# Optimization experiments

Hardware: AMD Instinct MI355X
Metric: run time of the kernel (lower is better)

The kernel has to match this reference:

```python
import jax, jax.numpy as jnp
import numpy as np

B, T, D_IN, D_H, D_OUT = 256, 512, 512, 1024, 512


def setup_inputs() -> dict:
    key = jax.random.key(0)
    k_x, k_wfc, k_bfc, k_wo, k_bo = jax.random.split(key, 5)
    # PyTorch Linear default init: U(-1/sqrt(fan_in), 1/sqrt(fan_in))
    lim_fc = 1.0 / np.sqrt(D_IN + D_H)
    lim_out = 1.0 / np.sqrt(D_H)
    return {
        "x": jax.random.normal(k_x, (B, T, D_IN), dtype=jnp.float32),
        "h": jnp.zeros((B, D_H), dtype=jnp.float32),
        "W_fc": jax.random.uniform(k_wfc, (D_H, D_IN + D_H), jnp.float32, -lim_fc, lim_fc),
        "b_fc": jax.random.uniform(k_bfc, (D_H,), jnp.float32, -lim_fc, lim_fc),
        "W_out": jax.random.uniform(k_wo, (D_OUT, D_H), jnp.float32, -lim_out, lim_out),
        "b_out": jax.random.uniform(k_bo, (D_OUT,), jnp.float32, -lim_out, lim_out),
    }


def reference(x, h, W_fc, b_fc, W_out, b_out):
    # x: [B, T, D_in], h: [B, D_h]
    xT = jnp.swapaxes(x, 0, 1)  # [T, B, D_in] for scan over time

    def step(h_t, x_t):
        combined = jnp.concatenate([x_t, h_t], axis=-1)  # [B, D_in + D_h]
        h_new = jnp.tanh(combined @ W_fc.T + b_fc)
        return h_new, None

    h_final, _ = jax.lax.scan(step, h, xT)
    y = h_final @ W_out.T + b_out  # [B, D_out]
    return (y, h_final)
```

## Files before the change

kernel.cpp:

```cpp
#include <hip/hip_runtime.h>
#include <hip/hip_bf16.h>
#include <math.h>

#define RNN_B    256
#define RNN_T    512
#define RNN_DIN  512
#define RNN_DH   1024
#define RNN_DOUT 512
#define RNN_K    (RNN_DIN + RNN_DH)

#define NGRP 16
#define MR   16
#define NBLK 16
#define NC   64

typedef __bf16 bf16x8 __attribute__((ext_vector_type(8)));
typedef float  f32x4  __attribute__((ext_vector_type(4)));
typedef unsigned long long u64;
typedef unsigned int u32;
typedef unsigned short u16;

static __device__ __forceinline__ bf16x8 ld_bf8(const __hip_bfloat16* p) {
  return *reinterpret_cast<const bf16x8*>(p);
}

static __device__ __forceinline__ bf16x8 ld_f32_as_bf8(const float* p) {
  const float4* q = reinterpret_cast<const float4*>(p);
  float4 u = q[0], v = q[1];
  bf16x8 r;
  r[0] = (__bf16)u.x; r[1] = (__bf16)u.y; r[2] = (__bf16)u.z; r[3] = (__bf16)u.w;
  r[4] = (__bf16)v.x; r[5] = (__bf16)v.y; r[6] = (__bf16)v.z; r[7] = (__bf16)v.w;
  return r;
}

__global__ void cast_f32_to_bf16(const float* __restrict__ src,
                                 unsigned long long* __restrict__ dst,
                                 int n4) {
  int i = blockIdx.x * blockDim.x + threadIdx.x;
  const int stride = gridDim.x * blockDim.x;
  for (; i < n4; i += stride) {
    float4 v = reinterpret_cast<const float4*>(src)[i];
    unsigned long long w =
        (unsigned long long)__builtin_bit_cast(unsigned short, (__bf16)v.x)
      | ((unsigned long long)__builtin_bit_cast(unsigned short, (__bf16)v.y) << 16)
      | ((unsigned long long)__builtin_bit_cast(unsigned short, (__bf16)v.z) << 32)
      | ((unsigned long long)__builtin_bit_cast(unsigned short, (__bf16)v.w) << 48);
    dst[i] = w;
  }
}

template<bool USE_XBF>
static __device__ __forceinline__ void xpart(const __hip_bfloat16* xbf, const float* xf,
                                             const __hip_bfloat16* Wbf,
                                             int m0, int nw, int lm, int lk, int t,
                                             f32x4* acc) {
#pragma unroll
  for (int i = 0; i < 4; ++i) acc[i] = (f32x4){0.f, 0.f, 0.f, 0.f};
  const __hip_bfloat16* Wr = Wbf + (size_t)(nw + lm) * RNN_K + lk;
  if constexpr (USE_XBF) {
    const __hip_bfloat16* xb = xbf + ((size_t)(m0 + lm) * RNN_T + (t - 1)) * RNN_DIN + lk;
#pragma unroll
    for (int s = 0; s < 16; ++s) {
      bf16x8 a = ld_bf8(xb + s * 32);
      bf16x8 b = ld_bf8(Wr + s * 32);
      acc[s & 3] = __builtin_amdgcn_mfma_f32_16x16x32_bf16(a, b, acc[s & 3], 0, 0, 0);
    }
  } else {
    const float* xb = xf + ((size_t)(m0 + lm) * RNN_T + (t - 1)) * RNN_DIN + lk;
#pragma unroll
    for (int s = 0; s < 16; ++s) {
      bf16x8 a = ld_f32_as_bf8(xb + s * 32);
      bf16x8 b = ld_bf8(Wr + s * 32);
      acc[s & 3] = __builtin_amdgcn_mfma_f32_16x16x32_bf16(a, b, acc[s & 3], 0, 0, 0);
    }
  }
}

template<bool USE_XBF>
__launch_bounds__(256, 1)
__global__ void rnn_scan(const __hip_bfloat16* __restrict__ xbf,
                         const float* __restrict__ xf,
                         const __hip_bfloat16* __restrict__ Wbf,
                         const float* __restrict__ bfc,
                         u32* hbuf32,
                         unsigned int* flags,
                         float* __restrict__ outh)
{
  const int bid = blockIdx.x;
  const int g = bid >> 4;
  const int c = bid & 15;
  const int tid = threadIdx.x;
  const int w  = tid >> 6;
  const int l  = tid & 63;
  const int lm = l & 15;
  const int lk = (l >> 4) * 8;
  const int m0 = g * MR;
  const int nw = c * NC + w * 16;

  __shared__ __align__(16) u32 hls[MR * 516];
  __shared__ __align__(16) u16 ots[16 * 68];

  const float bv = bfc[nw + lm];
  const int rr = (l >> 4) * 4;
  unsigned int* myflags = flags + g * (RNN_T + 1);
  const __hip_bfloat16* Wrh = Wbf + (size_t)(nw + lm) * RNN_K + RNN_DIN + lk;

  f32x4 acc[4];
  xpart<USE_XBF>(xbf, xf, Wbf, m0, nw, lm, lk, 1, acc);

  for (int t = 1; t <= RNN_T; ++t) {
    if (t > 1) {
      if (tid == 0) {
        unsigned int* fp = myflags + (t - 1);
        int it = 0;
        while (__hip_atomic_load(fp, __ATOMIC_RELAXED, __HIP_MEMORY_SCOPE_AGENT)
               < (unsigned)NBLK) {
          __builtin_amdgcn_s_sleep(1);
          if (++it > 4000000) break;
        }
      }
      __syncthreads();
    }

    {
      const u32* hsrc = hbuf32 + (size_t)((t - 1) & 1) * 131072 + (size_t)m0 * 512;
      u32 stg[32];
#pragma unroll
      for (int i = 0; i < 32; ++i)
        stg[i] = __hip_atomic_load(hsrc + i * 256 + tid,
                                   __ATOMIC_RELAXED, __HIP_MEMORY_SCOPE_AGENT);
#pragma unroll
      for (int i = 0; i < 32; ++i) {
        const int n = i * 256 + tid;
        hls[(n >> 9) * 516 + (n & 511)] = stg[i];
      }
    }
    __syncthreads();

#pragma unroll
    for (int ks = 0; ks < 32; ++ks) {
      const bf16x8 a = *reinterpret_cast<const bf16x8*>(
          &hls[lm * 516 + ks * 16 + (l >> 4) * 4]);
      const bf16x8 b = ld_bf8(Wrh + ks * 32);
      acc[ks & 3] = __builtin_amdgcn_mfma_f32_16x16x32_bf16(a, b, acc[ks & 3], 0, 0, 0);
    }

#pragma unroll
    for (int q = 0; q < 4; ++q) {
      float s = acc[0][q] + acc[1][q] + acc[2][q] + acc[3][q] + bv;
      float e  = __expf(-2.0f * fabsf(s));
      float th = (1.0f - e) * __builtin_amdgcn_rcpf(1.0f + e);
      float v  = copysignf(th, s);
      ots[(rr + q) * 68 + w * 16 + lm] = __builtin_bit_cast(u16, (__bf16)v);
      if (t == RNN_T) outh[(size_t)(m0 + rr + q) * RNN_DH + nw + lm] = v;
    }
    __syncthreads();

    {
      const u32* ots32 = reinterpret_cast<const u32*>(ots);
      const int i = tid >> 4, j0 = (tid & 15) * 2;
      u32 v0 = ots32[i * 34 + j0];
      u32 v1 = ots32[i * 34 + j0 + 1];
      u32* hdst = hbuf32 + (size_t)(t & 1) * 131072 + (size_t)(m0 + i) * 512 + c * 32;
      u32 r0 = __hip_atomic_exchange(hdst + j0,     v0,
                                     __ATOMIC_RELAXED, __HIP_MEMORY_SCOPE_AGENT);
      u32 r1 = __hip_atomic_exchange(hdst + j0 + 1, v1,
                                     __ATOMIC_RELAXED, __HIP_MEMORY_SCOPE_AGENT);
      asm volatile("" :: "v"(r0), "v"(r1));
    }
    asm volatile("s_waitcnt vmcnt(0)" ::: "memory");
    __syncthreads();

    if (tid == 0)
      __hip_atomic_fetch_add(myflags + t, 1u,
                             __ATOMIC_RELAXED, __HIP_MEMORY_SCOPE_AGENT);

    if (t < RNN_T) xpart<USE_XBF>(xbf, xf, Wbf, m0, nw, lm, lk, t + 1, acc);
  }
}

__global__ void out_gemm_mfma(const __hip_bfloat16* __restrict__ hfin,
                              const __hip_bfloat16* __restrict__ Wob,
                              const float* __restrict__ bout,
                              float* __restrict__ y)
{
  const int mi = blockIdx.x >> 3;
  const int ni = blockIdx.x & 7;
  const int w = threadIdx.x >> 6, l = threadIdx.x & 63;
  const int lm = l & 15, lk = (l >> 4) * 8;
  const int row0 = mi * 64 + w * 16;
  const int col0 = ni * 64;

  f32x4 acc[4];
#pragma unroll
  for (int i = 0; i < 4; ++i) acc[i] = (f32x4){0.f, 0.f, 0.f, 0.f};

#pragma unroll 4
  for (int ks = 0; ks < 32; ++ks) {
    bf16x8 a = ld_bf8(hfin + (size_t)(row0 + lm) * RNN_DH + ks * 32 + lk);
#pragma unroll
    for (int nf = 0; nf < 4; ++nf) {
      bf16x8 b = ld_bf8(Wob + (size_t)(col0 + nf * 16 + lm) * RNN_DH + ks * 32 + lk);
      acc[nf] = __builtin_amdgcn_mfma_f32_16x16x32_bf16(a, b, acc[nf], 0, 0, 0);
    }
  }
  const int rr = (l >> 4) * 4;
#pragma unroll
  for (int nf = 0; nf < 4; ++nf)
#pragma unroll
    for (int q = 0; q < 4; ++q)
      y[(size_t)(row0 + rr + q) * RNN_DOUT + col0 + nf * 16 + lm] =
          acc[nf][q] + bout[col0 + nf * 16 + lm];
}

__global__ void out_gemm(const float* __restrict__ hfin, const float* __restrict__ Wout,
                         const float* __restrict__ bout, float* __restrict__ y) {
  __shared__ float hs[RNN_DH];
  const int b = blockIdx.x;
  for (int j = threadIdx.x; j < RNN_DH; j += 256)
    hs[j] = hfin[(size_t)b * RNN_DH + j];
  __syncthreads();
  for (int o = threadIdx.x; o < RNN_DOUT; o += 256) {
    const float4* wr = reinterpret_cast<const float4*>(Wout + (size_t)o * RNN_DH);
    float acc = 0.f;
#pragma unroll 4
    for (int k4 = 0; k4 < RNN_DH / 4; ++k4) {
      float4 wv = wr[k4];
      acc += hs[4*k4] * wv.x + hs[4*k4+1] * wv.y + hs[4*k4+2] * wv.z + hs[4*k4+3] * wv.w;
    }
    y[(size_t)b * RNN_DOUT + o] = acc + bout[o];
  }
}

extern "C" void kernel_launch(void* const* d_in, const int* in_sizes, int n_in,
                              void* d_out, int out_size, void* d_ws, size_t ws_size,
                              hipStream_t stream) {
  const float* x    = (const float*)d_in[0];
  const float* h0   = (const float*)d_in[1];
  const float* Wfc  = (const float*)d_in[2];
  const float* bfc  = (const float*)d_in[3];
  const float* Wout = (const float*)d_in[4];
  const float* bout = (const float*)d_in[5];

  float* y    = (float*)d_out;
  float* outh = y + (size_t)RNN_B * RNN_DOUT;

  char* p = (char*)d_ws;
  __hip_bfloat16* hbuf = (__hip_bfloat16*)p;  p += (size_t)2 * RNN_B * RNN_DH * 2;
  unsigned int*   flags = (unsigned int*)p;   p += 65536;
  __hip_bfloat16* Wbf  = (__hip_bfloat16*)p;  p += (size_t)RNN_DH * RNN_K * 2;
  __hip_bfloat16* Wob  = (__hip_bfloat16*)p;
  const size_t need_wob = (size_t)(p - (char*)d_ws) + (size_t)RNN_DOUT * RNN_DH * 2;
  p += (size_t)RNN_DOUT * RNN_DH * 2;
  __hip_bfloat16* xbf  = (__hip_bfloat16*)p;
  const size_t need_xbf = (size_t)(p - (char*)d_ws) + (size_t)RNN_B * RNN_T * RNN_DIN * 2;
  const bool use_wob = (ws_size >= need_wob);
  const bool use_xbf = (ws_size >= need_xbf);

  hipMemsetAsync(flags, 0, NGRP * (RNN_T + 1) * sizeof(unsigned int), stream);

  cast_f32_to_bf16<<<dim3(1024), dim3(256), 0, stream>>>(
      Wfc, (unsigned long long*)Wbf, RNN_DH * RNN_K / 4);
  cast_f32_to_bf16<<<dim3(256), dim3(256), 0, stream>>>(
      h0, (unsigned long long*)hbuf, RNN_B * RNN_DH / 4);
  if (use_wob)
    cast_f32_to_bf16<<<dim3(256), dim3(256), 0, stream>>>(
        Wout, (unsigned long long*)Wob, RNN_DOUT * RNN_DH / 4);
  if (use_xbf)
    cast_f32_to_bf16<<<dim3(2048), dim3(256), 0, stream>>>(
        x, (unsigned long long*)xbf, RNN_B * RNN_T * RNN_DIN / 4);

  u32* hbuf32 = (u32*)hbuf;
  void* kargs[] = { (void*)&xbf, (void*)&x, (void*)&Wbf, (void*)&bfc,
                    (void*)&hbuf32, (void*)&flags, (void*)&outh };
  if (use_xbf) {
    hipLaunchCooperativeKernel((const void*)&rnn_scan<true>,
                               dim3(256), dim3(256), kargs, 0, stream);
  } else {
    hipLaunchCooperativeKernel((const void*)&rnn_scan<false>,
                               dim3(256), dim3(256), kargs, 0, stream);
  }

  if (use_wob) {
    out_gemm_mfma<<<dim3(32), dim3(256), 0, stream>>>(hbuf, Wob, bout, y);
  } else {
    out_gemm<<<dim3(256), dim3(256), 0, stream>>>(outh, Wout, bout, y);
  }
}
```

Measured before the change: 3.204 ms.

## Remove barriers in RNN step via per-wave spin, double-buffered LDS, shuffle packing

Each step now has every thread poll the readiness flag itself, so the barrier after the spin is gone. The LDS h tile is double-buffered by timestep parity so the next step's fill cannot overwrite data still being read. The output staging through LDS is replaced by a lane-pair shuffle that packs two bf16 values, and the even lanes then write them straight to global memory. This cuts two __syncthreads per step from the serial recurrence, at the cost of more polling traffic and more scattered atomic exchanges.

```diff
diff --git a/kernel.cpp b/kernel.cpp
--- a/kernel.cpp
+++ b/kernel.cpp
@@ -16,7 +16,6 @@
 
 typedef __bf16 bf16x8 __attribute__((ext_vector_type(8)));
 typedef float  f32x4  __attribute__((ext_vector_type(4)));
-typedef unsigned long long u64;
 typedef unsigned int u32;
 typedef unsigned short u16;
 
@@ -97,8 +96,7 @@
   const int m0 = g * MR;
   const int nw = c * NC + w * 16;
 
-  __shared__ __align__(16) u32 hls[MR * 516];
-  __shared__ __align__(16) u16 ots[16 * 68];
+  __shared__ __align__(16) u32 hls[2][MR * 516];
 
   const float bv = bfc[nw + lm];
   const int rr = (l >> 4) * 4;
@@ -110,16 +108,14 @@
 
   for (int t = 1; t <= RNN_T; ++t) {
     if (t > 1) {
-      if (tid == 0) {
-        unsigned int* fp = myflags + (t - 1);
-        int it = 0;
-        while (__hip_atomic_load(fp, __ATOMIC_RELAXED, __HIP_MEMORY_SCOPE_AGENT)
-               < (unsigned)NBLK) {
-          __builtin_amdgcn_s_sleep(1);
-          if (++it > 4000000) break;
-        }
+      unsigned int* fp = myflags + (t - 1);
+      int it = 0;
+      while (__hip_atomic_load(fp, __ATOMIC_RELAXED, __HIP_MEMORY_SCOPE_AGENT)
+             < (unsigned)NBLK) {
+        __builtin_amdgcn_s_sleep(1);
+        if (++it > 4000000) break;
       }
-      __syncthreads();
+      asm volatile("" ::: "memory");
     }
 
     {
@@ -132,7 +128,7 @@
 #pragma unroll
       for (int i = 0; i < 32; ++i) {
         const int n = i * 256 + tid;
-        hls[(n >> 9) * 516 + (n & 511)] = stg[i];
+        hls[t & 1][(n >> 9) * 516 + (n & 511)] = stg[i];
       }
     }
     __syncthreads();
@@ -140,33 +136,33 @@
 #pragma unroll
     for (int ks = 0; ks < 32; ++ks) {
       const bf16x8 a = *reinterpret_cast<const bf16x8*>(
-          &hls[lm * 516 + ks * 16 + (l >> 4) * 4]);
+          &hls[t & 1][lm * 516 + ks * 16 + (l >> 4) * 4]);
       const bf16x8 b = ld_bf8(Wrh + ks * 32);
       acc[ks & 3] = __builtin_amdgcn_mfma_f32_16x16x32_bf16(a, b, acc[ks & 3], 0, 0, 0);
     }
 
+    u32 hw[4];
 #pragma unroll
     for (int q = 0; q < 4; ++q) {
       float s = acc[0][q] + acc[1][q] + acc[2][q] + acc[3][q] + bv;
       float e  = __expf(-2.0f * fabsf(s));
       float th = (1.0f - e) * __builtin_amdgcn_rcpf(1.0f + e);
       float v  = copysignf(th, s);
-      ots[(rr + q) * 68 + w * 16 + lm] = __builtin_bit_cast(u16, (__bf16)v);
+      u32 my = (u32)__builtin_bit_cast(u16, (__bf16)v);
+      u32 pb = (u32)__shfl_xor((int)my, 1);
+      hw[q] = my | (pb << 16);
       if (t == RNN_T) outh[(size_t)(m0 + rr + q) * RNN_DH + nw + lm] = v;
     }
-    __syncthreads();
-
-    {
-      const u32* ots32 = reinterpret_cast<const u32*>(ots);
-      const int i = tid >> 4, j0 = (tid & 15) * 2;
-      u32 v0 = ots32[i * 34 + j0];
-      u32 v1 = ots32[i * 34 + j0 + 1];
-      u32* hdst = hbuf32 + (size_t)(t & 1) * 131072 + (size_t)(m0 + i) * 512 + c * 32;
-      u32 r0 = __hip_atomic_exchange(hdst + j0,     v0,
-                                     __ATOMIC_RELAXED, __HIP_MEMORY_SCOPE_AGENT);
-      u32 r1 = __hip_atomic_exchange(hdst + j0 + 1, v1,
-                                     __ATOMIC_RELAXED, __HIP_MEMORY_SCOPE_AGENT);
-      asm volatile("" :: "v"(r0), "v"(r1));
+
+    if (!(l & 1)) {
+      u32* hdst = hbuf32 + (size_t)(t & 1) * 131072
+                  + (size_t)(m0 + rr) * 512 + c * 32 + w * 8 + (lm >> 1);
+#pragma unroll
+      for (int q = 0; q < 4; ++q) {
+        u32 r0 = __hip_atomic_exchange(hdst + (size_t)q * 512, hw[q],
+                                       __ATOMIC_RELAXED, __HIP_MEMORY_SCOPE_AGENT);
+        asm volatile("" :: "v"(r0));
+      }
     }
     asm volatile("s_waitcnt vmcnt(0)" ::: "memory");
     __syncthreads();
```

Measured after the change: 5.390 ms. 68.2% more time.
